# Optimization experiments

Measured on AMD Instinct MI355X. Metric: run time of the kernel, lower is better.

Reference implementation:

```python
import jax, jax.numpy as jnp
import numpy as np

N, CH_IN, H, W = 4, 96, 128, 256
SF = 4  # scale_factor


def _conv(x, w, b):
    # 3x3 conv, stride 1, padding 1 ('SAME'), NCHW/OIHW layout
    y = jax.lax.conv_general_dilated(x, w, (1, 1), 'SAME',
                                     dimension_numbers=('NCHW', 'OIHW', 'NCHW'))
    return y + b[None, :, None, None]


def setup_inputs() -> dict:
    key = jax.random.key(0)
    ks = jax.random.split(key, 6)
    flow = jax.random.normal(ks[0], (N, 2, H, W), dtype=jnp.float32)
    feat = jax.random.normal(ks[1], (N, CH_IN, H, W), dtype=jnp.float32)
    # conv1: ch_in -> 128, conv2: 128 -> sf^2 * 9 = 144
    w1 = jax.random.normal(ks[2], (128, CH_IN, 3, 3), dtype=jnp.float32) * 0.05
    b1 = jax.random.normal(ks[3], (128,), dtype=jnp.float32) * 0.05
    w2 = jax.random.normal(ks[4], (SF * SF * 9, 128, 3, 3), dtype=jnp.float32) * 0.05
    b2 = jax.random.normal(ks[5], (SF * SF * 9,), dtype=jnp.float32) * 0.05
    return {'flow': flow, 'feat': feat, 'w1': w1, 'b1': b1, 'w2': w2, 'b2': b2}


def reference(flow, feat, w1, b1, w2, b2):
    n, _, h, w = flow.shape
    # convs: conv+LeakyReLU(0.1), then plain conv; mask scaled by 0.25
    hfeat = jax.nn.leaky_relu(_conv(feat, w1, b1), negative_slope=0.1)
    mask = 0.25 * _conv(hfeat, w2, b2)                      # (N, 144, H, W)
    # softmax over the 9 kernel positions
    m = mask.reshape(n, 9, SF, SF, h, w)                    # (N,9,4,4,H,W)
    m = jax.nn.softmax(m, axis=1)
    # unfold(4*flow, [3,3], padding=1): 9 shifted copies, row-major (ki,kj)
    fp = jnp.pad(4.0 * flow, ((0, 0), (0, 0), (1, 1), (1, 1)))
    patches = jnp.stack([fp[:, :, i:i + h, j:j + w]
                         for i in range(3) for j in range(3)], axis=2)  # (N,2,9,H,W)
    # convex combination over the 9 neighbors
    up = jnp.einsum('nkabhw,nckhw->ncabhw', m, patches)     # (N,2,4,4,H,W)
    up = up.transpose(0, 1, 4, 2, 5, 3)                     # (N,2,H,4,W,4)
    return up.reshape(n, 2, SF * h, SF * w)
```

## Files before the change

### kernel.cpp

```cpp
#include <hip/hip_runtime.h>
#include <hip/hip_bf16.h>

#define NN  4
#define CIN 96
#define C1  128
#define C2  144
#define HH  128
#define WW  256
#define NPX ((size_t)NN * HH * WW)

typedef short bf16x8 __attribute__((ext_vector_type(8)));
typedef float f32x4  __attribute__((ext_vector_type(4)));
typedef unsigned int u32x4 __attribute__((ext_vector_type(4)));

__device__ __forceinline__ short f2bs(float v) {
    __hip_bfloat16 b = __float2bfloat16(v);
    short s; __builtin_memcpy(&s, &b, 2); return s;
}

__device__ __forceinline__ void gld16(const void* g, void* l) {
    __builtin_amdgcn_global_load_lds(
        (const __attribute__((address_space(1))) void*)g,
        (__attribute__((address_space(3))) void*)l, 16, 0, 0);
}

__global__ __launch_bounds__(256) void prolog(
    const float* __restrict__ feat, short* __restrict__ featT,
    short* __restrict__ zbuf,
    const float* __restrict__ w1, short* __restrict__ w1p,
    const float* __restrict__ w2, short* __restrict__ w2p)
{
    __shared__ unsigned int lds[48 * 258];
    const int b   = blockIdx.x;
    const int tid = threadIdx.x;

    if (b < 512) {
        const int h = b & (HH - 1);
        const int n = b >> 7;
        if (b == 0 && tid < 32) zbuf[tid] = 0;

        #pragma unroll 4
        for (int cp = 0; cp < 48; ++cp) {
            float v0 = feat[(((size_t)n * CIN + 2 * cp    ) * HH + h) * WW + tid];
            float v1 = feat[(((size_t)n * CIN + 2 * cp + 1) * HH + h) * WW + tid];
            unsigned int p = (unsigned int)(unsigned short)f2bs(v0)
                           | ((unsigned int)(unsigned short)f2bs(v1) << 16);
            lds[cp * 258 + tid] = p;
        }
        __syncthreads();
        const size_t rowbase = (size_t)(n * HH + h) * WW * 32;
        #pragma unroll
        for (int kc = 0; kc < 3; ++kc) {
            short* dst = featT + (size_t)kc * (NPX * 32) + rowbase;
            #pragma unroll
            for (int it = 0; it < 4; ++it) {
                const int slot = it * 256 + tid;
                const int px = slot >> 2, sub = slot & 3;
                u32x4 v;
                #pragma unroll
                for (int k = 0; k < 4; ++k)
                    v[k] = lds[(kc * 16 + sub * 4 + k) * 258 + px];
                *(u32x4*)&dst[(size_t)slot * 8] = v;
            }
        }
        return;
    }

    const float* w; short* wp; int cin, nct, i;
    if (b < 944) { w = w1; wp = w1p; cin = CIN; nct = 8; i = (b - 512) * 256 + tid; }
    else         { w = w2; wp = w2p; cin = C1;  nct = 9; i = (b - 944) * 256 + tid; }
    const int j    = i & 7;
    const int col  = (i >> 3) & 15;
    const int quad = (i >> 7) & 3;
    int t = i >> 9;
    const int ct  = t % nct;  t /= nct;
    const int tap = t % 9;
    const int kci = t / 9;
    const int co = ct * 16 + col;
    const int ci = kci * 32 + quad * 8 + j;
    wp[i] = f2bs(w[((size_t)co * cin + ci) * 9 + tap]);
}

__global__ __launch_bounds__(256, 2) void conv1_mfma(
    const short* __restrict__ featT, const short* __restrict__ w1p,
    const float* __restrict__ b1, short* __restrict__ hfeat,
    const short* __restrict__ zbuf)
{
    __shared__ __attribute__((aligned(16))) short ldsA[3 * 258 * 32];
    __shared__ __attribute__((aligned(16))) short ldsB[3 * 8 * 512];
    const int tid  = threadIdx.x;
    const int bid  = ((blockIdx.x & 7) << 6) + (blockIdx.x >> 3);
    const int h    = bid & (HH - 1);
    const int n    = bid >> 7;
    const int lane = tid & 63, wave = tid >> 6;
    const int quad = lane >> 4, col = lane & 15;
    const int wp0  = wave * 64;

    f32x4 acc[4][8];
    #pragma unroll
    for (int mt = 0; mt < 4; ++mt)
        #pragma unroll
        for (int ct = 0; ct < 8; ++ct)
            #pragma unroll
            for (int r = 0; r < 4; ++r) acc[mt][ct][r] = 0.f;

    auto stageA = [&](int kci) {
        const short* cbase = featT + (size_t)kci * (NPX * 32);
        for (int s = tid; s < 3 * 258 * 4; s += 256) {
            const int cig = s & 3;
            const int px  = (s >> 2) % 258;
            const int row = (s >> 2) / 258;
            const int hh = h + row - 1, gw = px - 1;
            const short* g = zbuf;
            if (hh >= 0 && hh < HH && gw >= 0 && gw < WW)
                g = cbase + ((size_t)(n * HH + hh) * WW + gw) * 32
                    + ((cig ^ ((px >> 1) & 3)) << 3);
            gld16(g, &ldsA[s * 8]);
        }
    };
    auto stageB = [&](int kci, int tg) {
        const short* gB = w1p + (((size_t)(kci * 9 + tg * 3) * 8) << 9);
        for (int t = tid; t < 3 * 8 * 64; t += 256)
            gld16(gB + t * 8, &ldsB[t * 8]);
    };
    auto compute = [&](int tg) {
        __builtin_amdgcn_s_setprio(1);
        #pragma unroll
        for (int dw = 0; dw < 3; ++dw) {
            bf16x8 af[4];
            #pragma unroll
            for (int mt = 0; mt < 4; ++mt) {
                const int px = wp0 + mt * 16 + col + dw;
                const int slot = (tg * 258 + px) * 4 + (quad ^ ((px >> 1) & 3));
                af[mt] = *(const bf16x8*)&ldsA[slot * 8];
            }
            #pragma unroll
            for (int ct = 0; ct < 8; ++ct) {
                const bf16x8 bfr = *(const bf16x8*)&ldsB[((dw * 8 + ct) << 9) + (lane << 3)];
                #pragma unroll
                for (int mt = 0; mt < 4; ++mt)
                    acc[mt][ct] = __builtin_amdgcn_mfma_f32_16x16x32_bf16(af[mt], bfr, acc[mt][ct], 0, 0, 0);
            }
        }
        __builtin_amdgcn_s_setprio(0);
    };

    stageA(0);
    stageB(0, 0);
    __syncthreads();
    for (int kci = 0; kci < 3; ++kci)
        for (int tg = 0; tg < 3; ++tg) {
            compute(tg);
            __syncthreads();
            if (!(kci == 2 && tg == 2)) {
                int nk = kci, ntg = tg + 1;
                if (ntg == 3) { nk = kci + 1; ntg = 0; }
                if (ntg == 0) stageA(nk);
                stageB(nk, ntg);
                __syncthreads();
            }
        }

    float bias[8];
    #pragma unroll
    for (int ct = 0; ct < 8; ++ct) bias[ct] = b1[ct * 16 + col];
    #pragma unroll
    for (int mt = 0; mt < 4; ++mt)
        #pragma unroll
        for (int r = 0; r < 4; ++r) {
            const int w = wp0 + mt * 16 + quad * 4 + r;
            const size_t pxw = (size_t)(n * HH + h) * WW + w;
            #pragma unroll
            for (int ct = 0; ct < 8; ++ct) {
                float a = acc[mt][ct][r] + bias[ct];
                a = a > 0.f ? a : 0.1f * a;
                hfeat[((size_t)(ct >> 1) * NPX + pxw) * 32 + (ct & 1) * 16 + col] = f2bs(a);
            }
        }
}

__global__ __launch_bounds__(256, 2) void conv2_fused(
    const short* __restrict__ hfeat, const short* __restrict__ w2p,
    const float* __restrict__ b2, const float* __restrict__ flow,
    float* __restrict__ out, const short* __restrict__ zbuf)
{
    __shared__ __attribute__((aligned(16))) short ldsA[3 * 258 * 32];
    __shared__ __attribute__((aligned(16))) short ldsB[3 * 9 * 512];
    const int tid  = threadIdx.x;
    const int bid  = ((blockIdx.x & 7) << 6) + (blockIdx.x >> 3);
    const int h    = bid & (HH - 1);
    const int n    = bid >> 7;
    const int lane = tid & 63, wave = tid >> 6;
    const int quad = lane >> 4, col = lane & 15;
    const int wp0  = wave * 64;

    f32x4 acc[4][9];
    #pragma unroll
    for (int mt = 0; mt < 4; ++mt)
        #pragma unroll
        for (int ct = 0; ct < 9; ++ct)
            #pragma unroll
            for (int r = 0; r < 4; ++r) acc[mt][ct][r] = 0.f;

    auto stageA = [&](int kci) {
        const short* cbase = hfeat + (size_t)kci * (NPX * 32);
        for (int s = tid; s < 3 * 258 * 4; s += 256) {
            const int cig = s & 3;
            const int px  = (s >> 2) % 258;
            const int row = (s >> 2) / 258;
            const int hh = h + row - 1, gw = px - 1;
            const short* g = zbuf;
            if (hh >= 0 && hh < HH && gw >= 0 && gw < WW)
                g = cbase + ((size_t)(n * HH + hh) * WW + gw) * 32
                    + ((cig ^ ((px >> 1) & 3)) << 3);
            gld16(g, &ldsA[s * 8]);
        }
    };
    auto stageB = [&](int kci, int tg) {
        const short* gB = w2p + (((size_t)(kci * 9 + tg * 3) * 9) << 9);
        for (int t = tid; t < 3 * 9 * 64; t += 256)
            gld16(gB + t * 8, &ldsB[t * 8]);
    };
    auto compute = [&](int tg) {
        __builtin_amdgcn_s_setprio(1);
        #pragma unroll
        for (int dw = 0; dw < 3; ++dw) {
            bf16x8 af[4];
            #pragma unroll
            for (int mt = 0; mt < 4; ++mt) {
                const int px = wp0 + mt * 16 + col + dw;
                const int slot = (tg * 258 + px) * 4 + (quad ^ ((px >> 1) & 3));
                af[mt] = *(const bf16x8*)&ldsA[slot * 8];
            }
            #pragma unroll
            for (int ct = 0; ct < 9; ++ct) {
                const bf16x8 bfr = *(const bf16x8*)&ldsB[((dw * 9 + ct) << 9) + (lane << 3)];
                #pragma unroll
                for (int mt = 0; mt < 4; ++mt)
                    acc[mt][ct] = __builtin_amdgcn_mfma_f32_16x16x32_bf16(af[mt], bfr, acc[mt][ct], 0, 0, 0);
            }
        }
        __builtin_amdgcn_s_setprio(0);
    };

    stageA(0);
    stageB(0, 0);
    __syncthreads();
    for (int kci = 0; kci < 4; ++kci)
        for (int tg = 0; tg < 3; ++tg) {
            compute(tg);
            __syncthreads();
            if (!(kci == 3 && tg == 2)) {
                int nk = kci, ntg = tg + 1;
                if (ntg == 3) { nk = kci + 1; ntg = 0; }
                if (ntg == 0) stageA(nk);
                stageB(nk, ntg);
                __syncthreads();
            }
        }

    float* outs = (float*)ldsA;
    float* flds = (float*)ldsA + 8224;
    for (int i = tid; i < 2 * 3 * 258; i += 256) {
        const int px = i % 258;
        const int t  = i / 258;
        const int row = t % 3, c = t / 3;
        const int hh = h + row - 1, gw = px - 1;
        float v = 0.f;
        if (hh >= 0 && hh < HH && gw >= 0 && gw < WW)
            v = flow[(((size_t)n * 2 + c) * HH + hh) * WW + gw];
        flds[(c * 3 + row) * 264 + px] = v;
    }
    __syncthreads();

    const int a_ = col >> 2, b_ = col & 3;
    float bias[9];
    #pragma unroll
    for (int k = 0; k < 9; ++k) bias[k] = b2[k * 16 + col];

    #pragma unroll
    for (int mt = 0; mt < 4; ++mt) {
        const int w0 = wp0 + mt * 16 + quad * 4;
        float fw[2][3][6];
        #pragma unroll
        for (int c = 0; c < 2; ++c)
            #pragma unroll
            for (int ki = 0; ki < 3; ++ki)
                #pragma unroll
                for (int j = 0; j < 6; ++j)
                    fw[c][ki][j] = flds[(c * 3 + ki) * 264 + w0 + j];
        #pragma unroll
        for (int r = 0; r < 4; ++r) {
            const int w = w0 + r;
            float v[9], mx = -1e30f;
            #pragma unroll
            for (int k = 0; k < 9; ++k) {
                v[k] = 0.25f * (acc[mt][k][r] + bias[k]);
                mx = fmaxf(mx, v[k]);
            }
            float s = 0.f;
            #pragma unroll
            for (int k = 0; k < 9; ++k) { v[k] = __expf(v[k] - mx); s += v[k]; }
            const float inv = 4.f / s;
            float o0 = 0.f, o1 = 0.f;
            #pragma unroll
            for (int ki = 0; ki < 3; ++ki)
                #pragma unroll
                for (int kj = 0; kj < 3; ++kj) {
                    const float wgt = v[ki * 3 + kj];
                    o0 += wgt * fw[0][ki][r + kj];
                    o1 += wgt * fw[1][ki][r + kj];
                }
            outs[(0 * 4 + a_) * 1028 + 4 * w + b_] = o0 * inv;
            outs[(1 * 4 + a_) * 1028 + 4 * w + b_] = o1 * inv;
        }
    }
    __syncthreads();

    const int H4 = 4 * HH, W4 = 4 * WW;
    #pragma unroll
    for (int it = 0; it < 32; ++it) {
        const int i = it * 256 + tid;
        const int w4 = i & 1023, a = (i >> 10) & 3, c = i >> 12;
        out[(((size_t)(n * 2 + c)) * H4 + 4 * h + a) * W4 + w4] =
            outs[(c * 4 + a) * 1028 + w4];
    }
}

extern "C" void kernel_launch(void* const* d_in, const int* in_sizes, int n_in,
                              void* d_out, int out_size, void* d_ws, size_t ws_size,
                              hipStream_t stream)
{
    const float* flow = (const float*)d_in[0];
    const float* feat = (const float*)d_in[1];
    const float* w1   = (const float*)d_in[2];
    const float* b1   = (const float*)d_in[3];
    const float* w2   = (const float*)d_in[4];
    const float* b2   = (const float*)d_in[5];
    float* out = (float*)d_out;

    short* featT = (short*)d_ws;
    short* hfeat = featT + (size_t)3 * NPX * 32;
    short* w1p   = hfeat + (size_t)4 * NPX * 32;
    short* w2p   = w1p + (size_t)3 * 9 * 8 * 512;
    short* zbuf  = w2p + (size_t)4 * 9 * 9 * 512;

    prolog<<<1592, 256, 0, stream>>>(feat, featT, zbuf, w1, w1p, w2, w2p);
    conv1_mfma<<<NN * HH, 256, 0, stream>>>(featT, w1p, b1, hfeat, zbuf);
    conv2_fused<<<NN * HH, 256, 0, stream>>>(hfeat, w2p, b2, flow, out, zbuf);
}
```

Baseline: 176.9 us.

## Pipeline per-tap weight staging with triple-buffered LDS and vmcnt waits

Both conv kernels now load weights one tap at a time into a three-slot LDS ring, prefetching two taps ahead. Partial s_waitcnt vmcnt counts plus raw s_barrier replace the full __syncthreads pairs, so weight loads overlap MFMA compute instead of stalling the whole block at each stage. Input-row staging still happens every 9 taps behind a barrier. The per-wave vmcnt counts depend on exactly how many loads each wave issues, so a miscount could cause races, and the finer-grained steps add more barriers.

```diff
diff --git a/kernel.cpp b/kernel.cpp
--- a/kernel.cpp
+++ b/kernel.cpp
@@ -87,7 +87,7 @@
     const short* __restrict__ zbuf)
 {
     __shared__ __attribute__((aligned(16))) short ldsA[3 * 258 * 32];
-    __shared__ __attribute__((aligned(16))) short ldsB[3 * 8 * 512];
+    __shared__ __attribute__((aligned(16))) short ldsB[3][8 * 512];
     const int tid  = threadIdx.x;
     const int bid  = ((blockIdx.x & 7) << 6) + (blockIdx.x >> 3);
     const int h    = bid & (HH - 1);
@@ -118,48 +118,56 @@
             gld16(g, &ldsA[s * 8]);
         }
     };
-    auto stageB = [&](int kci, int tg) {
-        const short* gB = w1p + (((size_t)(kci * 9 + tg * 3) * 8) << 9);
-        for (int t = tid; t < 3 * 8 * 64; t += 256)
-            gld16(gB + t * 8, &ldsB[t * 8]);
-    };
-    auto compute = [&](int tg) {
+    auto stageB = [&](int q, int buf) {
+        const short* gB = w1p + (size_t)q * 4096;
+        #pragma unroll
+        for (int t = 0; t < 2; ++t)
+            gld16(gB + (t * 256 + tid) * 8, &ldsB[buf][(t * 256 + tid) * 8]);
+    };
+    auto compute = [&](int q) {
+        const int tap = q % 9, dh = tap / 3, dw = tap % 3;
+        const short* Bbuf = ldsB[q % 3];
         __builtin_amdgcn_s_setprio(1);
-        #pragma unroll
-        for (int dw = 0; dw < 3; ++dw) {
-            bf16x8 af[4];
-            #pragma unroll
-            for (int mt = 0; mt < 4; ++mt) {
-                const int px = wp0 + mt * 16 + col + dw;
-                const int slot = (tg * 258 + px) * 4 + (quad ^ ((px >> 1) & 3));
-                af[mt] = *(const bf16x8*)&ldsA[slot * 8];
-            }
-            #pragma unroll
-            for (int ct = 0; ct < 8; ++ct) {
-                const bf16x8 bfr = *(const bf16x8*)&ldsB[((dw * 8 + ct) << 9) + (lane << 3)];
-                #pragma unroll
-                for (int mt = 0; mt < 4; ++mt)
-                    acc[mt][ct] = __builtin_amdgcn_mfma_f32_16x16x32_bf16(af[mt], bfr, acc[mt][ct], 0, 0, 0);
-            }
+        bf16x8 af[4];
+        #pragma unroll
+        for (int mt = 0; mt < 4; ++mt) {
+            const int px = wp0 + mt * 16 + col + dw;
+            const int slot = (dh * 258 + px) * 4 + (quad ^ ((px >> 1) & 3));
+            af[mt] = *(const bf16x8*)&ldsA[slot * 8];
+        }
+        #pragma unroll
+        for (int ct = 0; ct < 8; ++ct) {
+            const bf16x8 bfr = *(const bf16x8*)&Bbuf[(ct << 9) + (lane << 3)];
+            #pragma unroll
+            for (int mt = 0; mt < 4; ++mt)
+                acc[mt][ct] = __builtin_amdgcn_mfma_f32_16x16x32_bf16(af[mt], bfr, acc[mt][ct], 0, 0, 0);
         }
         __builtin_amdgcn_s_setprio(0);
     };
 
     stageA(0);
     stageB(0, 0);
-    __syncthreads();
-    for (int kci = 0; kci < 3; ++kci)
-        for (int tg = 0; tg < 3; ++tg) {
-            compute(tg);
-            __syncthreads();
-            if (!(kci == 2 && tg == 2)) {
-                int nk = kci, ntg = tg + 1;
-                if (ntg == 3) { nk = kci + 1; ntg = 0; }
-                if (ntg == 0) stageA(nk);
-                stageB(nk, ntg);
-                __syncthreads();
-            }
-        }
+    stageB(1, 1);
+    __builtin_amdgcn_sched_barrier(0);
+    asm volatile("s_waitcnt vmcnt(2)" ::: "memory");
+    __builtin_amdgcn_s_barrier();
+    __builtin_amdgcn_sched_barrier(0);
+
+    for (int q = 0; q < 27; ++q) {
+        compute(q);
+        if (q == 26) break;
+        __builtin_amdgcn_sched_barrier(0);
+        if (q % 9 == 8) {
+            __builtin_amdgcn_s_barrier();
+            stageA(q / 9 + 1);
+        }
+        if (q + 2 <= 26) stageB(q + 2, (q + 2) % 3);
+        __builtin_amdgcn_sched_barrier(0);
+        if (q + 2 <= 26) asm volatile("s_waitcnt vmcnt(2)" ::: "memory");
+        else             asm volatile("s_waitcnt vmcnt(0)" ::: "memory");
+        __builtin_amdgcn_s_barrier();
+        __builtin_amdgcn_sched_barrier(0);
+    }
 
     float bias[8];
     #pragma unroll
@@ -185,7 +193,7 @@
     float* __restrict__ out, const short* __restrict__ zbuf)
 {
     __shared__ __attribute__((aligned(16))) short ldsA[3 * 258 * 32];
-    __shared__ __attribute__((aligned(16))) short ldsB[3 * 9 * 512];
+    __shared__ __attribute__((aligned(16))) short ldsB[3][9 * 512];
     const int tid  = threadIdx.x;
     const int bid  = ((blockIdx.x & 7) << 6) + (blockIdx.x >> 3);
     const int h    = bid & (HH - 1);
@@ -216,48 +224,60 @@
             gld16(g, &ldsA[s * 8]);
         }
     };
-    auto stageB = [&](int kci, int tg) {
-        const short* gB = w2p + (((size_t)(kci * 9 + tg * 3) * 9) << 9);
-        for (int t = tid; t < 3 * 9 * 64; t += 256)
-            gld16(gB + t * 8, &ldsB[t * 8]);
-    };
-    auto compute = [&](int tg) {
+    auto stageB = [&](int q, int buf) {
+        const short* gB = w2p + (size_t)q * 4608;
+        for (int t = tid; t < 576; t += 256)
+            gld16(gB + t * 8, &ldsB[buf][t * 8]);
+    };
+    auto waitB = [&](void) {
+        if (wave == 0) asm volatile("s_waitcnt vmcnt(3)" ::: "memory");
+        else           asm volatile("s_waitcnt vmcnt(2)" ::: "memory");
+    };
+    auto compute = [&](int q) {
+        const int tap = q % 9, dh = tap / 3, dw = tap % 3;
+        const short* Bbuf = ldsB[q % 3];
         __builtin_amdgcn_s_setprio(1);
-        #pragma unroll
-        for (int dw = 0; dw < 3; ++dw) {
-            bf16x8 af[4];
-            #pragma unroll
-            for (int mt = 0; mt < 4; ++mt) {
-                const int px = wp0 + mt * 16 + col + dw;
-                const int slot = (tg * 258 + px) * 4 + (quad ^ ((px >> 1) & 3));
-                af[mt] = *(const bf16x8*)&ldsA[slot * 8];
-            }
-            #pragma unroll
-            for (int ct = 0; ct < 9; ++ct) {
-                const bf16x8 bfr = *(const bf16x8*)&ldsB[((dw * 9 + ct) << 9) + (lane << 3)];
-                #pragma unroll
-                for (int mt = 0; mt < 4; ++mt)
-                    acc[mt][ct] = __builtin_amdgcn_mfma_f32_16x16x32_bf16(af[mt], bfr, acc[mt][ct], 0, 0, 0);
-            }
+        bf16x8 af[4];
+        #pragma unroll
+        for (int mt = 0; mt < 4; ++mt) {
+            const int px = wp0 + mt * 16 + col + dw;
+            const int slot = (dh * 258 + px) * 4 + (quad ^ ((px >> 1) & 3));
+            af[mt] = *(const bf16x8*)&ldsA[slot * 8];
+        }
+        #pragma unroll
+        for (int ct = 0; ct < 9; ++ct) {
+            const bf16x8 bfr = *(const bf16x8*)&Bbuf[(ct << 9) + (lane << 3)];
+            #pragma unroll
+            for (int mt = 0; mt < 4; ++mt)
+                acc[mt][ct] = __builtin_amdgcn_mfma_f32_16x16x32_bf16(af[mt], bfr, acc[mt][ct], 0, 0, 0);
         }
         __builtin_amdgcn_s_setprio(0);
     };
 
     stageA(0);
     stageB(0, 0);
+    stageB(1, 1);
+    __builtin_amdgcn_sched_barrier(0);
+    waitB();
+    __builtin_amdgcn_s_barrier();
+    __builtin_amdgcn_sched_barrier(0);
+
+    for (int q = 0; q < 36; ++q) {
+        compute(q);
+        if (q == 35) break;
+        __builtin_amdgcn_sched_barrier(0);
+        if (q % 9 == 8) {
+            __builtin_amdgcn_s_barrier();
+            stageA(q / 9 + 1);
+        }
+        if (q + 2 <= 35) stageB(q + 2, (q + 2) % 3);
+        __builtin_amdgcn_sched_barrier(0);
+        if (q + 2 <= 35) waitB();
+        else             asm volatile("s_waitcnt vmcnt(0)" ::: "memory");
+        __builtin_amdgcn_s_barrier();
+        __builtin_amdgcn_sched_barrier(0);
+    }
     __syncthreads();
-    for (int kci = 0; kci < 4; ++kci)
-        for (int tg = 0; tg < 3; ++tg) {
-            compute(tg);
-            __syncthreads();
-            if (!(kci == 3 && tg == 2)) {
-                int nk = kci, ntg = tg + 1;
-                if (ntg == 3) { nk = kci + 1; ntg = 0; }
-                if (ntg == 0) stageA(nk);
-                stageB(nk, ntg);
-                __syncthreads();
-            }
-        }
 
     float* outs = (float*)ldsA;
     float* flds = (float*)ldsA + 8224;
```

After: 178.5 us. No clear change (+0.9%).

## Process two output rows per conv1 block and stage all taps per channel chunk

Applied to the files above, without the earlier changes.

conv1 now uses 512-thread blocks covering two output rows, sharing a 4-row input halo in LDS and loading all 9 taps of weights per channel chunk at once. This cuts the number of barriers and the repeated loads of weights and halo rows, at the cost of more LDS per block (which may lower occupancy) and half as many blocks. It also removes the s_setprio hints from both conv kernels.

```diff
diff --git a/kernel.cpp b/kernel.cpp
--- a/kernel.cpp
+++ b/kernel.cpp
@@ -81,20 +81,21 @@
     wp[i] = f2bs(w[((size_t)co * cin + ci) * 9 + tap]);
 }
 
-__global__ __launch_bounds__(256, 2) void conv1_mfma(
+__global__ __launch_bounds__(512, 2) void conv1_mfma(
     const short* __restrict__ featT, const short* __restrict__ w1p,
     const float* __restrict__ b1, short* __restrict__ hfeat,
     const short* __restrict__ zbuf)
 {
-    __shared__ __attribute__((aligned(16))) short ldsA[3 * 258 * 32];
-    __shared__ __attribute__((aligned(16))) short ldsB[3 * 8 * 512];
+    __shared__ __attribute__((aligned(16))) short ldsA[4 * 258 * 32];
+    __shared__ __attribute__((aligned(16))) short ldsB[9 * 8 * 512];
     const int tid  = threadIdx.x;
-    const int bid  = ((blockIdx.x & 7) << 6) + (blockIdx.x >> 3);
-    const int h    = bid & (HH - 1);
-    const int n    = bid >> 7;
+    const int bid  = ((blockIdx.x & 7) << 5) + (blockIdx.x >> 3);
+    const int h0   = (bid & 63) * 2;
+    const int n    = bid >> 6;
     const int lane = tid & 63, wave = tid >> 6;
     const int quad = lane >> 4, col = lane & 15;
-    const int wp0  = wave * 64;
+    const int wr   = wave >> 2;
+    const int wp0  = (wave & 3) * 64;
 
     f32x4 acc[4][8];
     #pragma unroll
@@ -106,11 +107,11 @@
 
     auto stageA = [&](int kci) {
         const short* cbase = featT + (size_t)kci * (NPX * 32);
-        for (int s = tid; s < 3 * 258 * 4; s += 256) {
+        for (int s = tid; s < 4 * 258 * 4; s += 512) {
             const int cig = s & 3;
             const int px  = (s >> 2) % 258;
             const int row = (s >> 2) / 258;
-            const int hh = h + row - 1, gw = px - 1;
+            const int hh = h0 + row - 1, gw = px - 1;
             const short* g = zbuf;
             if (hh >= 0 && hh < HH && gw >= 0 && gw < WW)
                 g = cbase + ((size_t)(n * HH + hh) * WW + gw) * 32
@@ -118,52 +119,48 @@
             gld16(g, &ldsA[s * 8]);
         }
     };
-    auto stageB = [&](int kci, int tg) {
-        const short* gB = w1p + (((size_t)(kci * 9 + tg * 3) * 8) << 9);
-        for (int t = tid; t < 3 * 8 * 64; t += 256)
-            gld16(gB + t * 8, &ldsB[t * 8]);
-    };
-    auto compute = [&](int tg) {
-        __builtin_amdgcn_s_setprio(1);
+    auto stageB = [&](int kci) {
+        const short* gB = w1p + (size_t)kci * (9 * 8 * 512);
+        for (int s = tid; s < 4608; s += 512)
+            gld16(gB + s * 8, &ldsB[s * 8]);
+    };
+    auto compute3 = [&](int tg) {
         #pragma unroll
         for (int dw = 0; dw < 3; ++dw) {
             bf16x8 af[4];
             #pragma unroll
             for (int mt = 0; mt < 4; ++mt) {
                 const int px = wp0 + mt * 16 + col + dw;
-                const int slot = (tg * 258 + px) * 4 + (quad ^ ((px >> 1) & 3));
+                const int slot = ((wr + tg) * 258 + px) * 4 + (quad ^ ((px >> 1) & 3));
                 af[mt] = *(const bf16x8*)&ldsA[slot * 8];
             }
             #pragma unroll
             for (int ct = 0; ct < 8; ++ct) {
-                const bf16x8 bfr = *(const bf16x8*)&ldsB[((dw * 8 + ct) << 9) + (lane << 3)];
+                const bf16x8 bfr = *(const bf16x8*)
+                    &ldsB[(((tg * 3 + dw) * 8 + ct) << 9) + (lane << 3)];
                 #pragma unroll
                 for (int mt = 0; mt < 4; ++mt)
                     acc[mt][ct] = __builtin_amdgcn_mfma_f32_16x16x32_bf16(af[mt], bfr, acc[mt][ct], 0, 0, 0);
             }
         }
-        __builtin_amdgcn_s_setprio(0);
     };
 
     stageA(0);
-    stageB(0, 0);
+    stageB(0);
     __syncthreads();
-    for (int kci = 0; kci < 3; ++kci)
-        for (int tg = 0; tg < 3; ++tg) {
-            compute(tg);
-            __syncthreads();
-            if (!(kci == 2 && tg == 2)) {
-                int nk = kci, ntg = tg + 1;
-                if (ntg == 3) { nk = kci + 1; ntg = 0; }
-                if (ntg == 0) stageA(nk);
-                stageB(nk, ntg);
-                __syncthreads();
-            }
-        }
+    for (int kci = 0; kci < 3; ++kci) {
+        compute3(0); compute3(1); compute3(2);
+        if (kci == 2) break;
+        __syncthreads();
+        stageA(kci + 1);
+        stageB(kci + 1);
+        __syncthreads();
+    }
 
     float bias[8];
     #pragma unroll
     for (int ct = 0; ct < 8; ++ct) bias[ct] = b1[ct * 16 + col];
+    const int h = h0 + wr;
     #pragma unroll
     for (int mt = 0; mt < 4; ++mt)
         #pragma unroll
@@ -222,7 +219,6 @@
             gld16(gB + t * 8, &ldsB[t * 8]);
     };
     auto compute = [&](int tg) {
-        __builtin_amdgcn_s_setprio(1);
         #pragma unroll
         for (int dw = 0; dw < 3; ++dw) {
             bf16x8 af[4];
@@ -240,7 +236,6 @@
                     acc[mt][ct] = __builtin_amdgcn_mfma_f32_16x16x32_bf16(af[mt], bfr, acc[mt][ct], 0, 0, 0);
             }
         }
-        __builtin_amdgcn_s_setprio(0);
     };
 
     stageA(0);
@@ -346,6 +341,6 @@
     short* zbuf  = w2p + (size_t)4 * 9 * 9 * 512;
 
     prolog<<<1592, 256, 0, stream>>>(feat, featT, zbuf, w1, w1p, w2, w2p);
-    conv1_mfma<<<NN * HH, 256, 0, stream>>>(featT, w1p, b1, hfeat, zbuf);
+    conv1_mfma<<<NN * HH / 2, 512, 0, stream>>>(featT, w1p, b1, hfeat, zbuf);
     conv2_fused<<<NN * HH, 256, 0, stream>>>(hfeat, w2p, b2, flow, out, zbuf);
 }
```

Result: faster. 172.9 us (-2.3%).

## Read conv weights directly from global memory instead of staging through LDS

Applied to the files above, without the earlier changes.

Both conv kernels stop staging weight tiles into LDS. Each lane now loads its B fragments straight from global memory (L1/L2-cached), and all 9 taps of an input-channel group are computed between LDS refills, which cuts the number of barriers per block. The epilogue also reads flow values from LDS inside the inner loop instead of preloading them into a register array, which lowers register pressure. In exchange, every MFMA's B operand now depends on global-load latency with no double buffering, and the setprio hints are gone.

```diff
diff --git a/kernel.cpp b/kernel.cpp
--- a/kernel.cpp
+++ b/kernel.cpp
@@ -87,7 +87,6 @@
     const short* __restrict__ zbuf)
 {
     __shared__ __attribute__((aligned(16))) short ldsA[3 * 258 * 32];
-    __shared__ __attribute__((aligned(16))) short ldsB[3 * 8 * 512];
     const int tid  = threadIdx.x;
     const int bid  = ((blockIdx.x & 7) << 6) + (blockIdx.x >> 3);
     const int h    = bid & (HH - 1);
@@ -118,48 +117,35 @@
             gld16(g, &ldsA[s * 8]);
         }
     };
-    auto stageB = [&](int kci, int tg) {
-        const short* gB = w1p + (((size_t)(kci * 9 + tg * 3) * 8) << 9);
-        for (int t = tid; t < 3 * 8 * 64; t += 256)
-            gld16(gB + t * 8, &ldsB[t * 8]);
-    };
-    auto compute = [&](int tg) {
-        __builtin_amdgcn_s_setprio(1);
-        #pragma unroll
-        for (int dw = 0; dw < 3; ++dw) {
+
+    stageA(0);
+    __syncthreads();
+    for (int kci = 0; kci < 3; ++kci) {
+        #pragma unroll
+        for (int tap = 0; tap < 9; ++tap) {
+            const int dh = tap / 3, dw = tap % 3;
             bf16x8 af[4];
             #pragma unroll
             for (int mt = 0; mt < 4; ++mt) {
                 const int px = wp0 + mt * 16 + col + dw;
-                const int slot = (tg * 258 + px) * 4 + (quad ^ ((px >> 1) & 3));
+                const int slot = (dh * 258 + px) * 4 + (quad ^ ((px >> 1) & 3));
                 af[mt] = *(const bf16x8*)&ldsA[slot * 8];
             }
+            const short* bp = w1p + (((size_t)(kci * 9 + tap) * 8) << 9) + (lane << 3);
             #pragma unroll
             for (int ct = 0; ct < 8; ++ct) {
-                const bf16x8 bfr = *(const bf16x8*)&ldsB[((dw * 8 + ct) << 9) + (lane << 3)];
+                const bf16x8 bfr = *(const bf16x8*)(bp + ((size_t)ct << 9));
                 #pragma unroll
                 for (int mt = 0; mt < 4; ++mt)
                     acc[mt][ct] = __builtin_amdgcn_mfma_f32_16x16x32_bf16(af[mt], bfr, acc[mt][ct], 0, 0, 0);
             }
         }
-        __builtin_amdgcn_s_setprio(0);
-    };
-
-    stageA(0);
-    stageB(0, 0);
-    __syncthreads();
-    for (int kci = 0; kci < 3; ++kci)
-        for (int tg = 0; tg < 3; ++tg) {
-            compute(tg);
+        if (kci < 2) {
             __syncthreads();
-            if (!(kci == 2 && tg == 2)) {
-                int nk = kci, ntg = tg + 1;
-                if (ntg == 3) { nk = kci + 1; ntg = 0; }
-                if (ntg == 0) stageA(nk);
-                stageB(nk, ntg);
-                __syncthreads();
-            }
-        }
+            stageA(kci + 1);
+            __syncthreads();
+        }
+    }
 
     float bias[8];
     #pragma unroll
@@ -185,7 +171,6 @@
     float* __restrict__ out, const short* __restrict__ zbuf)
 {
     __shared__ __attribute__((aligned(16))) short ldsA[3 * 258 * 32];
-    __shared__ __attribute__((aligned(16))) short ldsB[3 * 9 * 512];
     const int tid  = threadIdx.x;
     const int bid  = ((blockIdx.x & 7) << 6) + (blockIdx.x >> 3);
     const int h    = bid & (HH - 1);
@@ -216,48 +201,36 @@
             gld16(g, &ldsA[s * 8]);
         }
     };
-    auto stageB = [&](int kci, int tg) {
-        const short* gB = w2p + (((size_t)(kci * 9 + tg * 3) * 9) << 9);
-        for (int t = tid; t < 3 * 9 * 64; t += 256)
-            gld16(gB + t * 8, &ldsB[t * 8]);
-    };
-    auto compute = [&](int tg) {
-        __builtin_amdgcn_s_setprio(1);
-        #pragma unroll
-        for (int dw = 0; dw < 3; ++dw) {
+
+    stageA(0);
+    __syncthreads();
+    for (int kci = 0; kci < 4; ++kci) {
+        #pragma unroll
+        for (int tap = 0; tap < 9; ++tap) {
+            const int dh = tap / 3, dw = tap % 3;
             bf16x8 af[4];
             #pragma unroll
             for (int mt = 0; mt < 4; ++mt) {
                 const int px = wp0 + mt * 16 + col + dw;
-                const int slot = (tg * 258 + px) * 4 + (quad ^ ((px >> 1) & 3));
+                const int slot = (dh * 258 + px) * 4 + (quad ^ ((px >> 1) & 3));
                 af[mt] = *(const bf16x8*)&ldsA[slot * 8];
             }
+            const short* bp = w2p + (((size_t)(kci * 9 + tap) * 9) << 9) + (lane << 3);
             #pragma unroll
             for (int ct = 0; ct < 9; ++ct) {
-                const bf16x8 bfr = *(const bf16x8*)&ldsB[((dw * 9 + ct) << 9) + (lane << 3)];
+                const bf16x8 bfr = *(const bf16x8*)(bp + ((size_t)ct << 9));
                 #pragma unroll
                 for (int mt = 0; mt < 4; ++mt)
                     acc[mt][ct] = __builtin_amdgcn_mfma_f32_16x16x32_bf16(af[mt], bfr, acc[mt][ct], 0, 0, 0);
             }
         }
-        __builtin_amdgcn_s_setprio(0);
-    };
-
-    stageA(0);
-    stageB(0, 0);
-    __syncthreads();
-    for (int kci = 0; kci < 4; ++kci)
-        for (int tg = 0; tg < 3; ++tg) {
-            compute(tg);
+        if (kci < 3) {
             __syncthreads();
-            if (!(kci == 3 && tg == 2)) {
-                int nk = kci, ntg = tg + 1;
-                if (ntg == 3) { nk = kci + 1; ntg = 0; }
-                if (ntg == 0) stageA(nk);
-                stageB(nk, ntg);
-                __syncthreads();
-            }
-        }
+            stageA(kci + 1);
+            __syncthreads();
+        }
+    }
+    __syncthreads();
 
     float* outs = (float*)ldsA;
     float* flds = (float*)ldsA + 8224;
@@ -281,14 +254,6 @@
     #pragma unroll
     for (int mt = 0; mt < 4; ++mt) {
         const int w0 = wp0 + mt * 16 + quad * 4;
-        float fw[2][3][6];
-        #pragma unroll
-        for (int c = 0; c < 2; ++c)
-            #pragma unroll
-            for (int ki = 0; ki < 3; ++ki)
-                #pragma unroll
-                for (int j = 0; j < 6; ++j)
-                    fw[c][ki][j] = flds[(c * 3 + ki) * 264 + w0 + j];
         #pragma unroll
         for (int r = 0; r < 4; ++r) {
             const int w = w0 + r;
@@ -308,8 +273,8 @@
                 #pragma unroll
                 for (int kj = 0; kj < 3; ++kj) {
                     const float wgt = v[ki * 3 + kj];
-                    o0 += wgt * fw[0][ki][r + kj];
-                    o1 += wgt * fw[1][ki][r + kj];
+                    o0 += wgt * flds[(0 * 3 + ki) * 264 + w + kj];
+                    o1 += wgt * flds[(1 * 3 + ki) * 264 + w + kj];
                 }
             outs[(0 * 4 + a_) * 1028 + 4 * w + b_] = o0 * inv;
             outs[(1 * 4 + a_) * 1028 + 4 * w + b_] = o1 * inv;
```

Result: slower. 223.2 us (+26.2%).
